# Optimization experiments

Measured on AMD Instinct MI355X. Metric: run time of the kernel, lower is better.

## Reference

```python
import jax, jax.numpy as jnp
import numpy as np

PI = float(np.pi)
LN_EPS = 1e-5
COS_EPS = 1e-6

D_HIDDEN, N_HEADS, D_HEAD, D_MLP = 1024, 16, 64, 4096
B, T = 4, 2048


def _xavier(key, shape):
    # torch xavier_uniform on 3D tensor: fan_in = shape[1]*shape[2]? torch uses
    # fan_in = shape[1] * receptive_field(shape[2:]), fan_out = shape[0] * rf.
    rf = 1
    for s in shape[2:]:
        rf *= s
    fan_in, fan_out = shape[1] * rf, shape[0] * rf
    bound = float(np.sqrt(6.0 / (fan_in + fan_out)))
    return jax.random.uniform(key, shape, jnp.float32, -bound, bound)


def setup_inputs() -> dict:
    key = jax.random.key(0)
    ks = jax.random.split(key, 10)
    x = jax.random.normal(ks[0], (B, T, D_HIDDEN), jnp.float32)
    W_Q = _xavier(ks[1], (N_HEADS, D_HIDDEN, 1))
    W_K = _xavier(ks[2], (N_HEADS, D_HIDDEN, 1))
    W_V = _xavier(ks[3], (N_HEADS, D_HIDDEN, D_HEAD))
    W_O = _xavier(ks[4], (D_HIDDEN, D_HEAD, N_HEADS))
    ln1_w = jnp.ones((D_HIDDEN,), jnp.float32)
    ln1_b = jnp.zeros((D_HIDDEN,), jnp.float32)
    ln2_w = jnp.ones((D_HIDDEN,), jnp.float32)
    ln2_b = jnp.zeros((D_HIDDEN,), jnp.float32)
    s1 = 1.0 / np.sqrt(D_HIDDEN)
    s2 = 1.0 / np.sqrt(D_MLP)
    W1 = jax.random.uniform(ks[5], (D_HIDDEN, D_MLP), jnp.float32, -s1, s1)
    b1 = jax.random.uniform(ks[6], (D_MLP,), jnp.float32, -s1, s1)
    W2 = jax.random.uniform(ks[7], (D_MLP, D_HIDDEN), jnp.float32, -s2, s2)
    b2 = jax.random.uniform(ks[8], (D_HIDDEN,), jnp.float32, -s2, s2)
    return {"x": x, "W_Q": W_Q, "W_K": W_K, "W_V": W_V, "W_O": W_O,
            "ln1_w": ln1_w, "ln1_b": ln1_b, "ln2_w": ln2_w, "ln2_b": ln2_b,
            "W1": W1, "b1": b1, "W2": W2, "b2": b2}


def _layer_norm(x, w, b):
    mu = jnp.mean(x, axis=-1, keepdims=True)
    var = jnp.mean(jnp.square(x - mu), axis=-1, keepdims=True)
    return (x - mu) * jax.lax.rsqrt(var + LN_EPS) * w + b


def _cos_attention(y, W_Q, W_K, W_V, W_O):
    q = jnp.einsum('btd,idh->btih', y, W_Q)  # (B,T,H,1)
    k = jnp.einsum('btd,idh->btih', y, W_K)  # (B,T,H,1)
    V = jnp.einsum('btd,idh->btih', y, W_V)  # (B,T,H,Dh)
    # use_tanh branch
    q = jnp.tanh(q) * (PI / 4)
    k = jnp.tanh(k) * (PI / 4)
    cos_k, sin_k = jnp.cos(k), jnp.sin(k)
    cos_KV = jnp.cumsum(cos_k * V, axis=1)
    sin_KV = jnp.cumsum(sin_k * V, axis=1)
    cos_Q, sin_Q = jnp.cos(q), jnp.sin(q)
    heads = cos_Q * cos_KV + sin_Q * sin_KV  # (B,T,H,Dh)
    # epsilon branch: normalizing denominator
    cos_K = jnp.cumsum(cos_k, axis=1)
    sin_K = jnp.cumsum(sin_k, axis=1)
    denom = cos_Q * cos_K + sin_Q * sin_K + COS_EPS  # (B,T,H,1)
    heads = heads / denom
    return jnp.einsum('dhi,btih->btd', W_O, heads)


def reference(x, W_Q, W_K, W_V, W_O, ln1_w, ln1_b, ln2_w, ln2_b, W1, b1, W2, b2):
    y = _layer_norm(x, ln1_w, ln1_b)
    x = x + _cos_attention(y, W_Q, W_K, W_V, W_O)
    y = _layer_norm(x, ln2_w, ln2_b)
    mlp = jnp.dot(jax.nn.gelu(jnp.dot(y, W1) + b1), W2) + b2
    return x + mlp
```

## Files before the change

### kernel.cpp

```cpp
#include <hip/hip_runtime.h>
#include <hip/hip_bf16.h>
#include <stdint.h>

typedef unsigned short u16;
typedef __attribute__((ext_vector_type(4))) unsigned int u32x4;
typedef __attribute__((ext_vector_type(8))) __bf16 bfx8;
typedef __attribute__((ext_vector_type(4))) float f32x4;

#define PI_F 3.14159265358979323846f

__device__ __forceinline__ float bf2f(u16 u) {
    unsigned v = ((unsigned)u) << 16; float f; __builtin_memcpy(&f, &v, 4); return f;
}
__device__ __forceinline__ u16 f2bf(float f) {
    unsigned u; __builtin_memcpy(&u, &f, 4);
    unsigned r = (u + 0x7fffu + ((u >> 16) & 1u)) >> 16; return (u16)r;
}

__device__ __forceinline__ void glds16(const u16* g, const u16* l) {
    __builtin_amdgcn_global_load_lds(
        (const __attribute__((address_space(1))) unsigned int*)(unsigned long long)g,
        (__attribute__((address_space(3))) unsigned int*)(unsigned int)(unsigned long long)l,
        16, 0, 0);
}

__global__ __launch_bounds__(256)
void tconv_kernel(const float* __restrict__ in, u16* __restrict__ out,
                  int R, int C, long inBatch, long outBatch)
{
    __shared__ float tile[64][65];
    const int tx = threadIdx.x & 63;
    const int ty = threadIdx.x >> 6;
    const int bc = blockIdx.x * 64;
    const int br = blockIdx.y * 64;
    const float* ip = in + (long)blockIdx.z * inBatch;
    u16* op = out + (long)blockIdx.z * outBatch;

    #pragma unroll
    for (int rr = ty; rr < 64; rr += 4) {
        int r = br + rr, c = bc + tx;
        tile[rr][tx] = (r < R && c < C) ? ip[(long)r * C + c] : 0.f;
    }
    __syncthreads();
    #pragma unroll
    for (int rr = ty; rr < 64; rr += 4) {
        int oc = bc + rr;
        int orr = br + tx;
        if (oc < C && orr < R)
            op[(long)oc * R + orr] = f2bf(tile[tx][rr]);
    }
}

template<bool DO_QK>
__global__ __launch_bounds__(256)
void ln_kernel(const float* __restrict__ X, const float* __restrict__ w,
               const float* __restrict__ b, u16* __restrict__ Ybf,
               const float* __restrict__ WQ, const float* __restrict__ WK,
               float* __restrict__ cqA, float* __restrict__ sqA,
               float* __restrict__ ckA, float* __restrict__ skA)
{
    __shared__ float yrow[1024];
    __shared__ float wsum[4], wsq[4];
    const int row = blockIdx.x;
    const int tid = threadIdx.x;
    const int lane = tid & 63;
    const int wv = tid >> 6;

    const float4 xv = ((const float4*)(X + (long)row * 1024))[tid];
    float s  = xv.x + xv.y + xv.z + xv.w;
    float sq = xv.x*xv.x + xv.y*xv.y + xv.z*xv.z + xv.w*xv.w;
    #pragma unroll
    for (int off = 32; off; off >>= 1) {
        s  += __shfl_down(s, off);
        sq += __shfl_down(sq, off);
    }
    if (lane == 0) { wsum[wv] = s; wsq[wv] = sq; }
    __syncthreads();
    const float ts = wsum[0] + wsum[1] + wsum[2] + wsum[3];
    const float tq = wsq[0] + wsq[1] + wsq[2] + wsq[3];
    const float mean = ts * (1.f / 1024.f);
    const float var  = tq * (1.f / 1024.f) - mean * mean;
    const float rstd = rsqrtf(var + 1e-5f);

    const float4 wv4 = ((const float4*)w)[tid];
    const float4 bv4 = ((const float4*)b)[tid];
    const float y0 = (xv.x - mean) * rstd * wv4.x + bv4.x;
    const float y1 = (xv.y - mean) * rstd * wv4.y + bv4.y;
    const float y2 = (xv.z - mean) * rstd * wv4.z + bv4.z;
    const float y3 = (xv.w - mean) * rstd * wv4.w + bv4.w;

    uint2 p;
    p.x = (unsigned)f2bf(y0) | ((unsigned)f2bf(y1) << 16);
    p.y = (unsigned)f2bf(y2) | ((unsigned)f2bf(y3) << 16);
    ((uint2*)(Ybf + (long)row * 1024))[tid] = p;

    if (DO_QK) {
        yrow[tid*4+0] = y0; yrow[tid*4+1] = y1;
        yrow[tid*4+2] = y2; yrow[tid*4+3] = y3;
        __syncthreads();
        #pragma unroll
        for (int i = 0; i < 4; ++i) {
            const int h = wv * 4 + i;
            const float* wqp = WQ + (long)h * 1024;
            const float* wkp = WK + (long)h * 1024;
            float dq = 0.f, dk = 0.f;
            #pragma unroll
            for (int j = 0; j < 16; ++j) {
                const float yv = yrow[lane + 64*j];
                dq = fmaf(yv, wqp[lane + 64*j], dq);
                dk = fmaf(yv, wkp[lane + 64*j], dk);
            }
            #pragma unroll
            for (int off = 32; off; off >>= 1) {
                dq += __shfl_down(dq, off);
                dk += __shfl_down(dk, off);
            }
            if (lane == 0) {
                const float aq = tanhf(dq) * (PI_F * 0.25f);
                const float ak = tanhf(dk) * (PI_F * 0.25f);
                float sv, cv;
                const long o = (long)h * 8192 + row;
                __sincosf(aq, &sv, &cv); cqA[o] = cv; sqA[o] = sv;
                __sincosf(ak, &sv, &cv); ckA[o] = cv; skA[o] = sv;
            }
        }
    }
}

__global__ __launch_bounds__(64)
void scan_kernel(const u16* __restrict__ V,
                 const float* __restrict__ cqA, const float* __restrict__ sqA,
                 const float* __restrict__ ckA, const float* __restrict__ skA,
                 u16* __restrict__ H)
{
    __shared__ u16 vt[64][64];
    __shared__ float lck[64], lsk[64], lrc[64], lrs[64];
    const int b = blockIdx.x >> 4;
    const int h = blockIdx.x & 15;
    const int lane = threadIdx.x;
    const long rowbase = (long)b * 2048;
    const long colbase = (long)h * 64;
    const long qbase = (long)h * 8192 + rowbase;

    float csum = 0.f, ssum = 0.f;
    float carry_c = 0.f, carry_s = 0.f;

    for (int ch = 0; ch < 32; ++ch) {
        const int t0 = ch * 64;
        __syncthreads();
        #pragma unroll
        for (int i = 0; i < 8; ++i) {
            const int tt = i * 8 + (lane >> 3);
            const int c0 = (lane & 7) * 8;
            *(u32x4*)&vt[tt][c0] =
                *(const u32x4*)(V + (rowbase + t0 + tt) * 1024 + colbase + c0);
        }
        {
            const float ck = ckA[qbase + t0 + lane];
            const float sk = skA[qbase + t0 + lane];
            const float cq = cqA[qbase + t0 + lane];
            const float sq = sqA[qbase + t0 + lane];
            float c = ck, sscan = sk;
            #pragma unroll
            for (int off = 1; off < 64; off <<= 1) {
                const float oc = __shfl_up(c, off);
                const float os = __shfl_up(sscan, off);
                if (lane >= off) { c += oc; sscan += os; }
            }
            const float cK = carry_c + c;
            const float sK = carry_s + sscan;
            carry_c += __shfl(c, 63);
            carry_s += __shfl(sscan, 63);
            const float denom = cq * cK + sq * sK + 1e-6f;
            lck[lane] = ck; lsk[lane] = sk;
            lrc[lane] = cq / denom; lrs[lane] = sq / denom;
        }
        __syncthreads();
        u16* outp = H + (rowbase + t0) * 1024 + colbase + lane;
        #pragma unroll 8
        for (int tt = 0; tt < 64; ++tt) {
            const float v = bf2f(vt[tt][lane]);
            csum = fmaf(lck[tt], v, csum);
            ssum = fmaf(lsk[tt], v, ssum);
            const float hv = lrc[tt] * csum + lrs[tt] * ssum;
            outp[(long)tt * 1024] = f2bf(hv);
        }
    }
}

template<int EPI>
__global__ __launch_bounds__(512, 2)
void gemm256(const u16* __restrict__ A, const u16* __restrict__ B,
             void* __restrict__ Cout, const float* __restrict__ res,
             const float* __restrict__ bias, int M, int N, int K, int nx)
{
    __shared__ u16 As[2 * 256 * 64];
    __shared__ u16 Bs[2 * 256 * 64];
    const int tid  = threadIdx.x;
    const int lane = tid & 63;
    const int wave = tid >> 6;
    const int wr = wave >> 2;
    const int wc = wave & 3;

    const int L = blockIdx.x;
    const int xcd = L & 7;
    const int qq = L >> 3;
    const int bx = qq % nx;
    const int by = (qq / nx) * 8 + xcd;
    const int brow = by * 256;
    const int bcol = bx * 256;

    const int srow8 = tid >> 3;
    const int chp   = tid & 7;
    const int clog  = (chp - (srow8 & 7)) & 7;
    const u16* Ag = A + (long)(brow + srow8) * K + clog * 8;
    const u16* Bg = B + (long)(bcol + srow8) * K + clog * 8;
    const long rowK64 = (long)64 * K;

    const int rr = lane & 15;
    const int kq = lane >> 4;
    const int lo0 = rr * 128 + ((kq + (rr & 7)) & 7) * 16;
    const int lo1 = rr * 128 + ((kq + 4 + (rr & 7)) & 7) * 16;
    const char* Ac = (const char*)As;
    const char* Bc = (const char*)Bs;
    const int aoff = wr * 16384;
    const int boff = (wc >> 1) * 16384 + (wc & 1) * 8192;

    f32x4 acc[8][4];
    #pragma unroll
    for (int i = 0; i < 8; ++i)
        #pragma unroll
        for (int j = 0; j < 4; ++j) acc[i][j] = (f32x4){0.f, 0.f, 0.f, 0.f};

    const int NT = K >> 6;

    #pragma unroll
    for (int q4 = 0; q4 < 4; ++q4) {
        glds16(Ag + (long)q4 * rowK64, &As[q4 * 4096 + tid * 8]);
        glds16(Bg + (long)q4 * rowK64, &Bs[q4 * 4096 + tid * 8]);
    }
    asm volatile("s_waitcnt vmcnt(0)" ::: "memory");
    asm volatile("s_barrier" ::: "memory");

    for (int t = 0; t < NT; ++t) {
        const int p  = t & 1;
        const int pn = p ^ 1;
        const long kofn = (long)((t + 1 < NT) ? (t + 1) : 0) * 64;
        const char* Ap = Ac + p * 32768;
        const char* Bp = Bc + p * 32768;

        bfx8 bA[8], bB0[4], bB1[4];

        #pragma unroll
        for (int m = 0; m < 4; ++m) {
            bA[m*2+0] = *(const bfx8*)(Ap + aoff + m * 2048 + lo0);
            bA[m*2+1] = *(const bfx8*)(Ap + aoff + m * 2048 + lo1);
        }
        #pragma unroll
        for (int n = 0; n < 2; ++n) {
            bB0[n*2+0] = *(const bfx8*)(Bp + boff + n * 2048 + lo0);
            bB0[n*2+1] = *(const bfx8*)(Bp + boff + n * 2048 + lo1);
        }
        #pragma unroll
        for (int q4 = 0; q4 < 4; ++q4)
            glds16(Ag + kofn + (long)q4 * rowK64,
                   &As[pn * 16384 + q4 * 4096 + tid * 8]);
        asm volatile("s_barrier" ::: "memory");
        asm volatile("s_waitcnt lgkmcnt(0)" ::: "memory");
        __builtin_amdgcn_sched_barrier(0);
        __builtin_amdgcn_s_setprio(1);
        #pragma unroll
        for (int m = 0; m < 4; ++m)
            #pragma unroll
            for (int n = 0; n < 2; ++n) {
                acc[m][n] = __builtin_amdgcn_mfma_f32_16x16x32_bf16(bA[m*2+0], bB0[n*2+0], acc[m][n], 0, 0, 0);
                acc[m][n] = __builtin_amdgcn_mfma_f32_16x16x32_bf16(bA[m*2+1], bB0[n*2+1], acc[m][n], 0, 0, 0);
            }
        __builtin_amdgcn_s_setprio(0);
        __builtin_amdgcn_sched_barrier(0);
        asm volatile("s_barrier" ::: "memory");

        #pragma unroll
        for (int n = 0; n < 2; ++n) {
            bB1[n*2+0] = *(const bfx8*)(Bp + boff + (2 + n) * 2048 + lo0);
            bB1[n*2+1] = *(const bfx8*)(Bp + boff + (2 + n) * 2048 + lo1);
        }
        #pragma unroll
        for (int q4 = 0; q4 < 4; ++q4)
            glds16(Bg + kofn + (long)q4 * rowK64,
                   &Bs[pn * 16384 + q4 * 4096 + tid * 8]);
        asm volatile("s_barrier" ::: "memory");
        asm volatile("s_waitcnt lgkmcnt(0)" ::: "memory");
        __builtin_amdgcn_sched_barrier(0);
        __builtin_amdgcn_s_setprio(1);
        #pragma unroll
        for (int m = 0; m < 4; ++m)
            #pragma unroll
            for (int n = 0; n < 2; ++n) {
                acc[m][2+n] = __builtin_amdgcn_mfma_f32_16x16x32_bf16(bA[m*2+0], bB1[n*2+0], acc[m][2+n], 0, 0, 0);
                acc[m][2+n] = __builtin_amdgcn_mfma_f32_16x16x32_bf16(bA[m*2+1], bB1[n*2+1], acc[m][2+n], 0, 0, 0);
            }
        __builtin_amdgcn_s_setprio(0);
        __builtin_amdgcn_sched_barrier(0);
        asm volatile("s_barrier" ::: "memory");

        #pragma unroll
        for (int m = 0; m < 4; ++m) {
            bA[m*2+0] = *(const bfx8*)(Ap + aoff + 8192 + m * 2048 + lo0);
            bA[m*2+1] = *(const bfx8*)(Ap + aoff + 8192 + m * 2048 + lo1);
        }
        asm volatile("s_barrier" ::: "memory");
        asm volatile("s_waitcnt lgkmcnt(0)" ::: "memory");
        __builtin_amdgcn_sched_barrier(0);
        __builtin_amdgcn_s_setprio(1);
        #pragma unroll
        for (int m = 0; m < 4; ++m)
            #pragma unroll
            for (int n = 0; n < 2; ++n) {
                acc[4+m][2+n] = __builtin_amdgcn_mfma_f32_16x16x32_bf16(bA[m*2+0], bB1[n*2+0], acc[4+m][2+n], 0, 0, 0);
                acc[4+m][2+n] = __builtin_amdgcn_mfma_f32_16x16x32_bf16(bA[m*2+1], bB1[n*2+1], acc[4+m][2+n], 0, 0, 0);
            }
        __builtin_amdgcn_s_setprio(0);
        __builtin_amdgcn_sched_barrier(0);
        asm volatile("s_barrier" ::: "memory");

        __builtin_amdgcn_s_setprio(1);
        #pragma unroll
        for (int m = 0; m < 4; ++m)
            #pragma unroll
            for (int n = 0; n < 2; ++n) {
                acc[4+m][n] = __builtin_amdgcn_mfma_f32_16x16x32_bf16(bA[m*2+0], bB0[n*2+0], acc[4+m][n], 0, 0, 0);
                acc[4+m][n] = __builtin_amdgcn_mfma_f32_16x16x32_bf16(bA[m*2+1], bB0[n*2+1], acc[4+m][n], 0, 0, 0);
            }
        __builtin_amdgcn_s_setprio(0);
        __builtin_amdgcn_sched_barrier(0);
        asm volatile("s_waitcnt vmcnt(0)" ::: "memory");
        asm volatile("s_barrier" ::: "memory");
    }

    const int crow0 = brow + wr * 128 + (lane >> 4) * 4;
    const int ccol0 = bcol + wc * 64 + rr;
    #pragma unroll
    for (int mi = 0; mi < 8; ++mi) {
        #pragma unroll
        for (int ni = 0; ni < 4; ++ni) {
            const int col = ccol0 + ni * 16;
            #pragma unroll
            for (int r = 0; r < 4; ++r) {
                const int row = crow0 + mi * 16 + r;
                const long idx = (long)row * N + col;
                const float v = acc[mi][ni][r];
                if (EPI == 0) {
                    ((u16*)Cout)[idx] = f2bf(v);
                } else if (EPI == 1) {
                    ((float*)Cout)[idx] = v + res[idx];
                } else if (EPI == 2) {
                    const float hh = v + bias[col];
                    const float z = 0.7978845608028654f * (hh + 0.044715f * hh * hh * hh);
                    const float e = __expf(2.f * z);
                    const float th = 1.f - 2.f / (e + 1.f);
                    ((u16*)Cout)[idx] = f2bf(0.5f * hh * (1.f + th));
                } else {
                    ((float*)Cout)[idx] = v + res[idx] + bias[col];
                }
            }
        }
    }
}

extern "C" void kernel_launch(void* const* d_in, const int* in_sizes, int n_in,
                              void* d_out, int out_size, void* d_ws, size_t ws_size,
                              hipStream_t stream)
{
    (void)in_sizes; (void)n_in; (void)out_size; (void)ws_size;
    const float* x    = (const float*)d_in[0];
    const float* WQ   = (const float*)d_in[1];
    const float* WK   = (const float*)d_in[2];
    const float* WV   = (const float*)d_in[3];
    const float* WO   = (const float*)d_in[4];
    const float* ln1w = (const float*)d_in[5];
    const float* ln1b = (const float*)d_in[6];
    const float* ln2w = (const float*)d_in[7];
    const float* ln2b = (const float*)d_in[8];
    const float* W1   = (const float*)d_in[9];
    const float* b1   = (const float*)d_in[10];
    const float* W2   = (const float*)d_in[11];
    const float* b2   = (const float*)d_in[12];
    float* out = (float*)d_out;

    char* ws = (char*)d_ws;
    u16*   Ybf  = (u16*)(ws + 0);
    u16*   Vbf  = (u16*)(ws + 16777216);
    u16*   Hbf  = (u16*)(ws + 33554432);
    float* X2   = (float*)(ws + 50331648);
    u16*   H1   = (u16*)(ws + 83886080);
    u16*   WVT  = (u16*)(ws + 150994944);
    u16*   WOT  = (u16*)(ws + 153092096);
    u16*   W1T  = (u16*)(ws + 155189248);
    u16*   W2T  = (u16*)(ws + 163577856);
    float* CQ   = (float*)(ws + 171966464);
    float* SQ   = (float*)(ws + 172490752);
    float* CK   = (float*)(ws + 173015040);
    float* SK   = (float*)(ws + 173539328);

    tconv_kernel<<<dim3(1, 16, 16), 256, 0, stream>>>(WV, WVT, 1024, 64, 1024L*64, 64L*1024);
    tconv_kernel<<<dim3(1, 1, 1024), 256, 0, stream>>>(WO, WOT, 64, 16, 1024L, 1024L);
    tconv_kernel<<<dim3(64, 16, 1), 256, 0, stream>>>(W1, W1T, 1024, 4096, 0L, 0L);
    tconv_kernel<<<dim3(16, 64, 1), 256, 0, stream>>>(W2, W2T, 4096, 1024, 0L, 0L);

    ln_kernel<true><<<8192, 256, 0, stream>>>(x, ln1w, ln1b, Ybf, WQ, WK, CQ, SQ, CK, SK);

    gemm256<0><<<128, 512, 0, stream>>>(Ybf, WVT, Vbf, nullptr, nullptr, 8192, 1024, 1024, 4);

    scan_kernel<<<64, 64, 0, stream>>>(Vbf, CQ, SQ, CK, SK, Hbf);

    gemm256<1><<<128, 512, 0, stream>>>(Hbf, WOT, X2, x, nullptr, 8192, 1024, 1024, 4);

    ln_kernel<false><<<8192, 256, 0, stream>>>(X2, ln2w, ln2b, Ybf,
                                               nullptr, nullptr, nullptr, nullptr, nullptr, nullptr);

    gemm256<2><<<512, 512, 0, stream>>>(Ybf, W1T, H1, nullptr, b1, 8192, 4096, 1024, 16);

    gemm256<3><<<128, 512, 0, stream>>>(H1, W2T, out, X2, b2, 8192, 1024, 4096, 4);
}
```

Baseline: 576.0 us.

## Parallelize scan across time chunks and use 256x128 GEMM tiles for N=1024

The causal scan kernel now uses 8 waves per (batch, head). Each wave first reduces its 256-step chunk, then adds carries from the earlier chunks before doing the local scan, replacing a single wave walking all 2048 steps. The GEMM is rewritten with a BN template parameter and finer interleaving of A/B staging with partial vmcnt waits. The N=1024 GEMMs use 256x128 tiles, doubling the grid to 256 blocks so more CUs are busy. The scan reads V twice and gives up LDS reuse, and the narrower tiles lower arithmetic intensity.

```diff
diff --git a/kernel.cpp b/kernel.cpp
--- a/kernel.cpp
+++ b/kernel.cpp
@@ -127,241 +127,289 @@
     }
 }
 
-__global__ __launch_bounds__(64)
+__global__ __launch_bounds__(512)
 void scan_kernel(const u16* __restrict__ V,
                  const float* __restrict__ cqA, const float* __restrict__ sqA,
                  const float* __restrict__ ckA, const float* __restrict__ skA,
                  u16* __restrict__ H)
 {
-    __shared__ u16 vt[64][64];
-    __shared__ float lck[64], lsk[64], lrc[64], lrs[64];
+    __shared__ float totcV[8][64], totsV[8][64];
+    __shared__ float totc[8], tots[8];
     const int b = blockIdx.x >> 4;
     const int h = blockIdx.x & 15;
-    const int lane = threadIdx.x;
+    const int wv = threadIdx.x >> 6;
+    const int lane = threadIdx.x & 63;
     const long rowbase = (long)b * 2048;
-    const long colbase = (long)h * 64;
     const long qbase = (long)h * 8192 + rowbase;
-
-    float csum = 0.f, ssum = 0.f;
-    float carry_c = 0.f, carry_s = 0.f;
-
-    for (int ch = 0; ch < 32; ++ch) {
-        const int t0 = ch * 64;
-        __syncthreads();
-        #pragma unroll
-        for (int i = 0; i < 8; ++i) {
-            const int tt = i * 8 + (lane >> 3);
-            const int c0 = (lane & 7) * 8;
-            *(u32x4*)&vt[tt][c0] =
-                *(const u32x4*)(V + (rowbase + t0 + tt) * 1024 + colbase + c0);
-        }
-        {
-            const float ck = ckA[qbase + t0 + lane];
-            const float sk = skA[qbase + t0 + lane];
-            const float cq = cqA[qbase + t0 + lane];
-            const float sq = sqA[qbase + t0 + lane];
-            float c = ck, sscan = sk;
-            #pragma unroll
-            for (int off = 1; off < 64; off <<= 1) {
-                const float oc = __shfl_up(c, off);
-                const float os = __shfl_up(sscan, off);
-                if (lane >= off) { c += oc; sscan += os; }
-            }
-            const float cK = carry_c + c;
-            const float sK = carry_s + sscan;
-            carry_c += __shfl(c, 63);
-            carry_s += __shfl(sscan, 63);
-            const float denom = cq * cK + sq * sK + 1e-6f;
-            lck[lane] = ck; lsk[lane] = sk;
-            lrc[lane] = cq / denom; lrs[lane] = sq / denom;
-        }
-        __syncthreads();
-        u16* outp = H + (rowbase + t0) * 1024 + colbase + lane;
-        #pragma unroll 8
-        for (int tt = 0; tt < 64; ++tt) {
-            const float v = bf2f(vt[tt][lane]);
-            csum = fmaf(lck[tt], v, csum);
-            ssum = fmaf(lsk[tt], v, ssum);
-            const float hv = lrc[tt] * csum + lrs[tt] * ssum;
-            outp[(long)tt * 1024] = f2bf(hv);
-        }
-    }
-}
-
-template<int EPI>
+    const int t0 = wv * 256;
+
+    const u16* vp = V + (rowbase + t0) * 1024 + (long)h * 64 + lane;
+
+    float tc = 0.f, ts = 0.f, kc = 0.f, ks = 0.f;
+    #pragma unroll 4
+    for (int tt = 0; tt < 256; ++tt) {
+        const float ck = ckA[qbase + t0 + tt];
+        const float sk = skA[qbase + t0 + tt];
+        const float vx = bf2f(vp[(long)tt * 1024]);
+        tc = fmaf(ck, vx, tc); ts = fmaf(sk, vx, ts);
+        kc += ck; ks += sk;
+    }
+    totcV[wv][lane] = tc; totsV[wv][lane] = ts;
+    if (lane == 0) { totc[wv] = kc; tots[wv] = ks; }
+    __syncthreads();
+
+    float carC = 0.f, carS = 0.f, carKc = 0.f, carKs = 0.f;
+    for (int w2 = 0; w2 < wv; ++w2) {
+        carC += totcV[w2][lane]; carS += totsV[w2][lane];
+        carKc += totc[w2]; carKs += tots[w2];
+    }
+
+    float csum = carC, ssum = carS, kcs = carKc, kss = carKs;
+    u16* outp = H + (rowbase + t0) * 1024 + (long)h * 64 + lane;
+    #pragma unroll 4
+    for (int tt = 0; tt < 256; ++tt) {
+        const long qo = qbase + t0 + tt;
+        const float ck = ckA[qo], sk = skA[qo];
+        const float cq = cqA[qo], sq2 = sqA[qo];
+        const float vx = bf2f(vp[(long)tt * 1024]);
+        csum = fmaf(ck, vx, csum); ssum = fmaf(sk, vx, ssum);
+        kcs += ck; kss += sk;
+        const float denom = cq * kcs + sq2 * kss + 1e-6f;
+        const float hv = (cq * csum + sq2 * ssum) / denom;
+        outp[(long)tt * 1024] = f2bf(hv);
+    }
+}
+
+template<int EPI, int BN>
 __global__ __launch_bounds__(512, 2)
-void gemm256(const u16* __restrict__ A, const u16* __restrict__ B,
-             void* __restrict__ Cout, const float* __restrict__ res,
-             const float* __restrict__ bias, int M, int N, int K, int nx)
+void gemm5(const u16* __restrict__ A, const u16* __restrict__ B,
+           void* __restrict__ Cout, const float* __restrict__ res,
+           const float* __restrict__ bias, int N, int K, int nx)
 {
+    constexpr int NFR = BN / 64;
+    constexpr int BSTR = BN * 64;
     __shared__ u16 As[2 * 256 * 64];
-    __shared__ u16 Bs[2 * 256 * 64];
+    __shared__ u16 Bs[2 * BSTR];
+
     const int tid  = threadIdx.x;
     const int lane = tid & 63;
     const int wave = tid >> 6;
     const int wr = wave >> 2;
     const int wc = wave & 3;
+    const int rr = lane & 15;
+    const int kq = lane >> 4;
 
     const int L = blockIdx.x;
     const int xcd = L & 7;
     const int qq = L >> 3;
-    const int bx = qq % nx;
-    const int by = (qq / nx) * 8 + xcd;
-    const int brow = by * 256;
-    const int bcol = bx * 256;
-
-    const int srow8 = tid >> 3;
-    const int chp   = tid & 7;
-    const int clog  = (chp - (srow8 & 7)) & 7;
-    const u16* Ag = A + (long)(brow + srow8) * K + clog * 8;
-    const u16* Bg = B + (long)(bcol + srow8) * K + clog * 8;
-    const long rowK64 = (long)64 * K;
-
-    const int rr = lane & 15;
-    const int kq = lane >> 4;
-    const int lo0 = rr * 128 + ((kq + (rr & 7)) & 7) * 16;
-    const int lo1 = rr * 128 + ((kq + 4 + (rr & 7)) & 7) * 16;
-    const char* Ac = (const char*)As;
-    const char* Bc = (const char*)Bs;
-    const int aoff = wr * 16384;
-    const int boff = (wc >> 1) * 16384 + (wc & 1) * 8192;
-
-    f32x4 acc[8][4];
+    const int brow = ((qq / nx) * 8 + xcd) * 256;
+    const int bcol = (qq % nx) * BN;
+
+    const int v = tid >> 3;
+    const int chp = tid & 7;
+    const int clog = (chp - (v & 7)) & 7;
+    const u16* AgB = A + (long)(brow + v) * K + clog * 8;
+    const int rowB = (BN == 256) ? (v + (v & 32)) : v;
+    const u16* BgB = B + (long)(bcol + rowB) * K + clog * 8;
+    const long K64 = (long)64 * K;
+
+    const int ph0 = ((kq + (rr & 7)) & 7) * 16;
+    const int ph1 = ((kq + 4 + (rr & 7)) & 7) * 16;
+    const int arb = rr * 128;
+    const int aq0 = wr * 8192;
+    const int aq1 = (2 + wr) * 8192;
+    const int bq0 = (wc >> 1) * 8192 + (wc & 1) * 4096;
+    const int bq1 = (2 + (wc >> 1)) * 8192 + (wc & 1) * 4096;
+
+    f32x4 acc[8][NFR];
     #pragma unroll
     for (int i = 0; i < 8; ++i)
         #pragma unroll
-        for (int j = 0; j < 4; ++j) acc[i][j] = (f32x4){0.f, 0.f, 0.f, 0.f};
+        for (int j = 0; j < NFR; ++j) acc[i][j] = (f32x4){0.f, 0.f, 0.f, 0.f};
 
     const int NT = K >> 6;
-
-    #pragma unroll
-    for (int q4 = 0; q4 < 4; ++q4) {
-        glds16(Ag + (long)q4 * rowK64, &As[q4 * 4096 + tid * 8]);
-        glds16(Bg + (long)q4 * rowK64, &Bs[q4 * 4096 + tid * 8]);
+    const char* AsB = (const char*)As;
+    const char* BsB = (const char*)Bs;
+
+#define STAGE_A0(nb, kn) { glds16(AgB + (kn),             &As[(nb)*16384 + tid*8]); \
+                           glds16(AgB + (kn) + 2*K64,     &As[(nb)*16384 + 4096 + tid*8]); }
+#define STAGE_A1(nb, kn) { glds16(AgB + (kn) + K64,       &As[(nb)*16384 + 8192 + tid*8]); \
+                           glds16(AgB + (kn) + 3*K64,     &As[(nb)*16384 + 12288 + tid*8]); }
+#define STAGE_B0(nb, kn) { glds16(BgB + (kn),             &Bs[(nb)*16384 + tid*8]); \
+                           glds16(BgB + (kn) + 2*K64,     &Bs[(nb)*16384 + 4096 + tid*8]); }
+#define STAGE_B1(nb, kn) { glds16(BgB + (kn) + (K64>>1),  &Bs[(nb)*16384 + 8192 + tid*8]); \
+                           glds16(BgB + (kn) + (K64>>1) + 2*K64, &Bs[(nb)*16384 + 12288 + tid*8]); }
+#define STAGE_B128(nb, kn) { glds16(BgB + (kn),           &Bs[(nb)*8192 + tid*8]); \
+                             glds16(BgB + (kn) + K64,     &Bs[(nb)*8192 + 4096 + tid*8]); }
+#define BAR  asm volatile("s_barrier" ::: "memory")
+#define LGKM0 asm volatile("s_waitcnt lgkmcnt(0)" ::: "memory")
+#define SB __builtin_amdgcn_sched_barrier(0)
+
+    if constexpr (BN == 256) {
+        STAGE_A0(0, 0); STAGE_B0(0, 0); STAGE_B1(0, 0); STAGE_A1(0, 0);
+    } else {
+        STAGE_A0(0, 0); STAGE_B128(0, 0); STAGE_A1(0, 0);
     }
     asm volatile("s_waitcnt vmcnt(0)" ::: "memory");
-    asm volatile("s_barrier" ::: "memory");
+    BAR;
 
     for (int t = 0; t < NT; ++t) {
-        const int p  = t & 1;
-        const int pn = p ^ 1;
-        const long kofn = (long)((t + 1 < NT) ? (t + 1) : 0) * 64;
-        const char* Ap = Ac + p * 32768;
-        const char* Bp = Bc + p * 32768;
-
-        bfx8 bA[8], bB0[4], bB1[4];
-
-        #pragma unroll
-        for (int m = 0; m < 4; ++m) {
-            bA[m*2+0] = *(const bfx8*)(Ap + aoff + m * 2048 + lo0);
-            bA[m*2+1] = *(const bfx8*)(Ap + aoff + m * 2048 + lo1);
+        const int buf = t & 1, nb = buf ^ 1;
+        const long kn = (long)((t + 1 < NT) ? (t + 1) : 0) * 64;
+        const char* Ap = AsB + buf * 32768;
+        const char* Bp = BsB + buf * (BSTR * 2);
+
+        if constexpr (BN == 256) {
+            bfx8 a0[8], a1[8], b0[4], b1[4];
+            #pragma unroll
+            for (int mi = 0; mi < 4; ++mi) {
+                a0[mi*2+0] = *(const bfx8*)(Ap + aq0 + mi*2048 + arb + ph0);
+                a0[mi*2+1] = *(const bfx8*)(Ap + aq0 + mi*2048 + arb + ph1);
+            }
+            #pragma unroll
+            for (int nf = 0; nf < 2; ++nf) {
+                b0[nf*2+0] = *(const bfx8*)(Bp + bq0 + nf*2048 + arb + ph0);
+                b0[nf*2+1] = *(const bfx8*)(Bp + bq0 + nf*2048 + arb + ph1);
+            }
+            STAGE_A0(nb, kn);
+            BAR; LGKM0; SB;
+            __builtin_amdgcn_s_setprio(1);
+            #pragma unroll
+            for (int mi = 0; mi < 4; ++mi)
+                #pragma unroll
+                for (int nf = 0; nf < 2; ++nf) {
+                    acc[mi][nf] = __builtin_amdgcn_mfma_f32_16x16x32_bf16(a0[mi*2+0], b0[nf*2+0], acc[mi][nf], 0, 0, 0);
+                    acc[mi][nf] = __builtin_amdgcn_mfma_f32_16x16x32_bf16(a0[mi*2+1], b0[nf*2+1], acc[mi][nf], 0, 0, 0);
+                }
+            __builtin_amdgcn_s_setprio(0); SB;
+            asm volatile("s_waitcnt vmcnt(4)" ::: "memory");
+            BAR;
+            #pragma unroll
+            for (int nf = 0; nf < 2; ++nf) {
+                b1[nf*2+0] = *(const bfx8*)(Bp + bq1 + nf*2048 + arb + ph0);
+                b1[nf*2+1] = *(const bfx8*)(Bp + bq1 + nf*2048 + arb + ph1);
+            }
+            STAGE_B0(nb, kn);
+            BAR; LGKM0; SB;
+            __builtin_amdgcn_s_setprio(1);
+            #pragma unroll
+            for (int mi = 0; mi < 4; ++mi)
+                #pragma unroll
+                for (int nf = 0; nf < 2; ++nf) {
+                    acc[mi][2+nf] = __builtin_amdgcn_mfma_f32_16x16x32_bf16(a0[mi*2+0], b1[nf*2+0], acc[mi][2+nf], 0, 0, 0);
+                    acc[mi][2+nf] = __builtin_amdgcn_mfma_f32_16x16x32_bf16(a0[mi*2+1], b1[nf*2+1], acc[mi][2+nf], 0, 0, 0);
+                }
+            __builtin_amdgcn_s_setprio(0); SB;
+            asm volatile("s_waitcnt vmcnt(4)" ::: "memory");
+            BAR;
+            #pragma unroll
+            for (int mi = 0; mi < 4; ++mi) {
+                a1[mi*2+0] = *(const bfx8*)(Ap + aq1 + mi*2048 + arb + ph0);
+                a1[mi*2+1] = *(const bfx8*)(Ap + aq1 + mi*2048 + arb + ph1);
+            }
+            STAGE_B1(nb, kn);
+            BAR; LGKM0; SB;
+            __builtin_amdgcn_s_setprio(1);
+            #pragma unroll
+            for (int mi = 0; mi < 4; ++mi)
+                #pragma unroll
+                for (int nf = 0; nf < 2; ++nf) {
+                    acc[4+mi][2+nf] = __builtin_amdgcn_mfma_f32_16x16x32_bf16(a1[mi*2+0], b1[nf*2+0], acc[4+mi][2+nf], 0, 0, 0);
+                    acc[4+mi][2+nf] = __builtin_amdgcn_mfma_f32_16x16x32_bf16(a1[mi*2+1], b1[nf*2+1], acc[4+mi][2+nf], 0, 0, 0);
+                }
+            __builtin_amdgcn_s_setprio(0); SB;
+            BAR;
+            STAGE_A1(nb, kn);
+            BAR; SB;
+            __builtin_amdgcn_s_setprio(1);
+            #pragma unroll
+            for (int mi = 0; mi < 4; ++mi)
+                #pragma unroll
+                for (int nf = 0; nf < 2; ++nf) {
+                    acc[4+mi][nf] = __builtin_amdgcn_mfma_f32_16x16x32_bf16(a1[mi*2+0], b0[nf*2+0], acc[4+mi][nf], 0, 0, 0);
+                    acc[4+mi][nf] = __builtin_amdgcn_mfma_f32_16x16x32_bf16(a1[mi*2+1], b0[nf*2+1], acc[4+mi][nf], 0, 0, 0);
+                }
+            __builtin_amdgcn_s_setprio(0); SB;
+            asm volatile("s_waitcnt vmcnt(4)" ::: "memory");
+            BAR;
+        } else {
+            bfx8 a0[8], a1[8], bb[4];
+            #pragma unroll
+            for (int mi = 0; mi < 4; ++mi) {
+                a0[mi*2+0] = *(const bfx8*)(Ap + aq0 + mi*2048 + arb + ph0);
+                a0[mi*2+1] = *(const bfx8*)(Ap + aq0 + mi*2048 + arb + ph1);
+            }
+            #pragma unroll
+            for (int nf = 0; nf < 2; ++nf) {
+                bb[nf*2+0] = *(const bfx8*)(Bp + bq0 + nf*2048 + arb + ph0);
+                bb[nf*2+1] = *(const bfx8*)(Bp + bq0 + nf*2048 + arb + ph1);
+            }
+            STAGE_A0(nb, kn); STAGE_B128(nb, kn);
+            BAR; LGKM0; SB;
+            __builtin_amdgcn_s_setprio(1);
+            #pragma unroll
+            for (int mi = 0; mi < 4; ++mi)
+                #pragma unroll
+                for (int nf = 0; nf < 2; ++nf) {
+                    acc[mi][nf] = __builtin_amdgcn_mfma_f32_16x16x32_bf16(a0[mi*2+0], bb[nf*2+0], acc[mi][nf], 0, 0, 0);
+                    acc[mi][nf] = __builtin_amdgcn_mfma_f32_16x16x32_bf16(a0[mi*2+1], bb[nf*2+1], acc[mi][nf], 0, 0, 0);
+                }
+            __builtin_amdgcn_s_setprio(0); SB;
+            asm volatile("s_waitcnt vmcnt(4)" ::: "memory");
+            BAR;
+            #pragma unroll
+            for (int mi = 0; mi < 4; ++mi) {
+                a1[mi*2+0] = *(const bfx8*)(Ap + aq1 + mi*2048 + arb + ph0);
+                a1[mi*2+1] = *(const bfx8*)(Ap + aq1 + mi*2048 + arb + ph1);
+            }
+            STAGE_A1(nb, kn);
+            BAR; LGKM0; SB;
+            __builtin_amdgcn_s_setprio(1);
+            #pragma unroll
+            for (int mi = 0; mi < 4; ++mi)
+                #pragma unroll
+                for (int nf = 0; nf < 2; ++nf) {
+                    acc[4+mi][nf] = __builtin_amdgcn_mfma_f32_16x16x32_bf16(a1[mi*2+0], bb[nf*2+0], acc[4+mi][nf], 0, 0, 0);
+                    acc[4+mi][nf] = __builtin_amdgcn_mfma_f32_16x16x32_bf16(a1[mi*2+1], bb[nf*2+1], acc[4+mi][nf], 0, 0, 0);
+                }
+            __builtin_amdgcn_s_setprio(0); SB;
+            asm volatile("s_waitcnt vmcnt(2)" ::: "memory");
+            BAR;
         }
-        #pragma unroll
-        for (int n = 0; n < 2; ++n) {
-            bB0[n*2+0] = *(const bfx8*)(Bp + boff + n * 2048 + lo0);
-            bB0[n*2+1] = *(const bfx8*)(Bp + boff + n * 2048 + lo1);
-        }
-        #pragma unroll
-        for (int q4 = 0; q4 < 4; ++q4)
-            glds16(Ag + kofn + (long)q4 * rowK64,
-                   &As[pn * 16384 + q4 * 4096 + tid * 8]);
-        asm volatile("s_barrier" ::: "memory");
-        asm volatile("s_waitcnt lgkmcnt(0)" ::: "memory");
-        __builtin_amdgcn_sched_barrier(0);
-        __builtin_amdgcn_s_setprio(1);
-        #pragma unroll
-        for (int m = 0; m < 4; ++m)
-            #pragma unroll
-            for (int n = 0; n < 2; ++n) {
-                acc[m][n] = __builtin_amdgcn_mfma_f32_16x16x32_bf16(bA[m*2+0], bB0[n*2+0], acc[m][n], 0, 0, 0);
-                acc[m][n] = __builtin_amdgcn_mfma_f32_16x16x32_bf16(bA[m*2+1], bB0[n*2+1], acc[m][n], 0, 0, 0);
-            }
-        __builtin_amdgcn_s_setprio(0);
-        __builtin_amdgcn_sched_barrier(0);
-        asm volatile("s_barrier" ::: "memory");
-
-        #pragma unroll
-        for (int n = 0; n < 2; ++n) {
-            bB1[n*2+0] = *(const bfx8*)(Bp + boff + (2 + n) * 2048 + lo0);
-            bB1[n*2+1] = *(const bfx8*)(Bp + boff + (2 + n) * 2048 + lo1);
-        }
-        #pragma unroll
-        for (int q4 = 0; q4 < 4; ++q4)
-            glds16(Bg + kofn + (long)q4 * rowK64,
-                   &Bs[pn * 16384 + q4 * 4096 + tid * 8]);
-        asm volatile("s_barrier" ::: "memory");
-        asm volatile("s_waitcnt lgkmcnt(0)" ::: "memory");
-        __builtin_amdgcn_sched_barrier(0);
-        __builtin_amdgcn_s_setprio(1);
-        #pragma unroll
-        for (int m = 0; m < 4; ++m)
-            #pragma unroll
-            for (int n = 0; n < 2; ++n) {
-                acc[m][2+n] = __builtin_amdgcn_mfma_f32_16x16x32_bf16(bA[m*2+0], bB1[n*2+0], acc[m][2+n], 0, 0, 0);
-                acc[m][2+n] = __builtin_amdgcn_mfma_f32_16x16x32_bf16(bA[m*2+1], bB1[n*2+1], acc[m][2+n], 0, 0, 0);
-            }
-        __builtin_amdgcn_s_setprio(0);
-        __builtin_amdgcn_sched_barrier(0);
-        asm volatile("s_barrier" ::: "memory");
-
-        #pragma unroll
-        for (int m = 0; m < 4; ++m) {
-            bA[m*2+0] = *(const bfx8*)(Ap + aoff + 8192 + m * 2048 + lo0);
-            bA[m*2+1] = *(const bfx8*)(Ap + aoff + 8192 + m * 2048 + lo1);
-        }
-        asm volatile("s_barrier" ::: "memory");
-        asm volatile("s_waitcnt lgkmcnt(0)" ::: "memory");
-        __builtin_amdgcn_sched_barrier(0);
-        __builtin_amdgcn_s_setprio(1);
-        #pragma unroll
-        for (int m = 0; m < 4; ++m)
-            #pragma unroll
-            for (int n = 0; n < 2; ++n) {
-                acc[4+m][2+n] = __builtin_amdgcn_mfma_f32_16x16x32_bf16(bA[m*2+0], bB1[n*2+0], acc[4+m][2+n], 0, 0, 0);
-                acc[4+m][2+n] = __builtin_amdgcn_mfma_f32_16x16x32_bf16(bA[m*2+1], bB1[n*2+1], acc[4+m][2+n], 0, 0, 0);
-            }
-        __builtin_amdgcn_s_setprio(0);
-        __builtin_amdgcn_sched_barrier(0);
-        asm volatile("s_barrier" ::: "memory");
-
-        __builtin_amdgcn_s_setprio(1);
-        #pragma unroll
-        for (int m = 0; m < 4; ++m)
-            #pragma unroll
-            for (int n = 0; n < 2; ++n) {
-                acc[4+m][n] = __builtin_amdgcn_mfma_f32_16x16x32_bf16(bA[m*2+0], bB0[n*2+0], acc[4+m][n], 0, 0, 0);
-                acc[4+m][n] = __builtin_amdgcn_mfma_f32_16x16x32_bf16(bA[m*2+1], bB0[n*2+1], acc[4+m][n], 0, 0, 0);
-            }
-        __builtin_amdgcn_s_setprio(0);
-        __builtin_amdgcn_sched_barrier(0);
-        asm volatile("s_waitcnt vmcnt(0)" ::: "memory");
-        asm volatile("s_barrier" ::: "memory");
-    }
-
-    const int crow0 = brow + wr * 128 + (lane >> 4) * 4;
-    const int ccol0 = bcol + wc * 64 + rr;
+    }
+#undef STAGE_A0
+#undef STAGE_A1
+#undef STAGE_B0
+#undef STAGE_B1
+#undef STAGE_B128
+#undef BAR
+#undef LGKM0
+#undef SB
+
+    const int crow0 = brow + wr * 128 + kq * 4;
+    const int ccol0 = bcol + wc * (BN / 4) + rr;
     #pragma unroll
     for (int mi = 0; mi < 8; ++mi) {
         #pragma unroll
-        for (int ni = 0; ni < 4; ++ni) {
+        for (int ni = 0; ni < NFR; ++ni) {
             const int col = ccol0 + ni * 16;
             #pragma unroll
             for (int r = 0; r < 4; ++r) {
                 const int row = crow0 + mi * 16 + r;
                 const long idx = (long)row * N + col;
-                const float v = acc[mi][ni][r];
+                const float vvv = acc[mi][ni][r];
                 if (EPI == 0) {
-                    ((u16*)Cout)[idx] = f2bf(v);
+                    ((u16*)Cout)[idx] = f2bf(vvv);
                 } else if (EPI == 1) {
-                    ((float*)Cout)[idx] = v + res[idx];
+                    ((float*)Cout)[idx] = vvv + res[idx];
                 } else if (EPI == 2) {
-                    const float hh = v + bias[col];
+                    const float hh = vvv + bias[col];
                     const float z = 0.7978845608028654f * (hh + 0.044715f * hh * hh * hh);
                     const float e = __expf(2.f * z);
                     const float th = 1.f - 2.f / (e + 1.f);
                     ((u16*)Cout)[idx] = f2bf(0.5f * hh * (1.f + th));
                 } else {
-                    ((float*)Cout)[idx] = v + res[idx] + bias[col];
+                    ((float*)Cout)[idx] = vvv + res[idx] + bias[col];
                 }
             }
         }
@@ -410,16 +458,16 @@
 
     ln_kernel<true><<<8192, 256, 0, stream>>>(x, ln1w, ln1b, Ybf, WQ, WK, CQ, SQ, CK, SK);
 
-    gemm256<0><<<128, 512, 0, stream>>>(Ybf, WVT, Vbf, nullptr, nullptr, 8192, 1024, 1024, 4);
-
-    scan_kernel<<<64, 64, 0, stream>>>(Vbf, CQ, SQ, CK, SK, Hbf);
-
-    gemm256<1><<<128, 512, 0, stream>>>(Hbf, WOT, X2, x, nullptr, 8192, 1024, 1024, 4);
+    gemm5<0, 128><<<256, 512, 0, stream>>>(Ybf, WVT, Vbf, nullptr, nullptr, 1024, 1024, 8);
+
+    scan_kernel<<<64, 512, 0, stream>>>(Vbf, CQ, SQ, CK, SK, Hbf);
+
+    gemm5<1, 128><<<256, 512, 0, stream>>>(Hbf, WOT, X2, x, nullptr, 1024, 1024, 8);
 
     ln_kernel<false><<<8192, 256, 0, stream>>>(X2, ln2w, ln2b, Ybf,
                                                nullptr, nullptr, nullptr, nullptr, nullptr, nullptr);
 
-    gemm256<2><<<512, 512, 0, stream>>>(Ybf, W1T, H1, nullptr, b1, 8192, 4096, 1024, 16);
-
-    gemm256<3><<<128, 512, 0, stream>>>(H1, W2T, out, X2, b2, 8192, 1024, 4096, 4);
-}
+    gemm5<2, 256><<<512, 512, 0, stream>>>(Ybf, W1T, H1, nullptr, b1, 4096, 1024, 16);
+
+    gemm5<3, 128><<<256, 512, 0, stream>>>(H1, W2T, out, X2, b2, 1024, 4096, 8);
+}
```

Result: faster. 507.5 us (-11.9%).
